# Performance work log

Hardware: AMD Instinct MI355X
Metric: run time of the kernel (lower is better)

## Reference

```python
import jax, jax.numpy as jnp
import numpy as np

B, N, D = 8, 1024, 768
R, SH = 10, 2
H = R + SH            # 12 total heads
DH = D // H           # 64
DF = 2 * D            # FFN hidden


def _layernorm(x, g, b, eps=1e-5):
    mu = jnp.mean(x, axis=-1, keepdims=True)
    var = jnp.var(x, axis=-1, keepdims=True)
    return (x - mu) * jax.lax.rsqrt(var + eps) * g + b


def setup_inputs() -> dict:
    key = jax.random.key(0)
    ks = jax.random.split(key, 12)
    s = 0.02
    inp = {
        'nodes': jax.random.normal(ks[0], (B, N, D), dtype=jnp.float32),
        'relation_mask': jax.random.uniform(ks[1], (B, N, N, R), dtype=jnp.float32),
        'node_mask': jax.random.randint(ks[2], (B, N), 0, 2).astype(bool),
        'Wq': jax.random.normal(ks[3], (D, D), dtype=jnp.float32) * s,
        'bq': jnp.zeros((D,), jnp.float32),
        'Wk': jax.random.normal(ks[4], (D, D), dtype=jnp.float32) * s,
        'bk': jnp.zeros((D,), jnp.float32),
        'Wv': jax.random.normal(ks[5], (D, D), dtype=jnp.float32) * s,
        'bv': jnp.zeros((D,), jnp.float32),
        'Wo': jax.random.normal(ks[6], (D, D), dtype=jnp.float32) * s,
        'bo': jnp.zeros((D,), jnp.float32),
        'ln1_g': jnp.ones((D,), jnp.float32),
        'ln1_b': jnp.zeros((D,), jnp.float32),
        'W1': jax.random.normal(ks[7], (DF, D), dtype=jnp.float32) * s,
        'b1': jnp.zeros((DF,), jnp.float32),
        'W2': jax.random.normal(ks[8], (D, DF), dtype=jnp.float32) * s,
        'b2': jnp.zeros((D,), jnp.float32),
        'ln2_g': jnp.ones((D,), jnp.float32),
        'ln2_b': jnp.zeros((D,), jnp.float32),
    }
    return inp


def reference(nodes, relation_mask, node_mask, Wq, bq, Wk, bk, Wv, bv, Wo, bo,
              ln1_g, ln1_b, W1, b1, W2, b2, ln2_g, ln2_b):
    neg_inf = jnp.float32(-jnp.inf)
    # projections -> [B, H, N, DH]
    q = (nodes @ Wq.T + bq).reshape(B, N, H, DH).transpose(0, 2, 1, 3)
    k = (nodes @ Wk.T + bk).reshape(B, N, H, DH).transpose(0, 2, 1, 3)
    v = (nodes @ Wv.T + bv).reshape(B, N, H, DH).transpose(0, 2, 1, 3)
    scores = jnp.einsum('bhqd,bhkd->bhqk', q, k) / jnp.sqrt(jnp.float32(DH))
    # relation-typed gating on first R heads
    rel_gate = relation_mask.transpose(0, 3, 1, 2)          # [B, R, N, N]
    typed = jnp.where(rel_gate < 1e-4, neg_inf, scores[:, :R])
    scores = jnp.concatenate([typed, scores[:, R:]], axis=1)
    # key padding mask
    key_mask = node_mask[:, None, None, :]                  # [B,1,1,N]
    scores = jnp.where(key_mask, scores, neg_inf)
    attn = jax.nn.softmax(scores, axis=-1)
    attn = jnp.nan_to_num(attn, nan=0.0)                    # rows with no valid keys -> 0
    out = jnp.einsum('bhqk,bhkd->bhqd', attn, v)
    out = out.transpose(0, 2, 1, 3).reshape(B, N, D)
    out = out @ Wo.T + bo
    h = _layernorm(nodes + out, ln1_g, ln1_b)
    ffn = jax.nn.gelu(h @ W1.T + b1, approximate=False) @ W2.T + b2
    h = _layernorm(h + ffn, ln2_g, ln2_b)
    return h
```

## Files before the change

kernel.cpp:

```cpp
#include <hip/hip_runtime.h>
#include <stdint.h>
#include <math.h>

typedef unsigned short u16;
typedef __bf16 bf16x8 __attribute__((ext_vector_type(8)));
typedef unsigned short u16x8 __attribute__((ext_vector_type(8)));
typedef unsigned short us4 __attribute__((ext_vector_type(4)));
typedef float f32x4 __attribute__((ext_vector_type(4)));

#define DEVI __device__ __forceinline__

constexpr int B_ = 8, N_ = 1024, D_ = 768, H_ = 12, DH_ = 64, DF_ = 1536;

DEVI u16 f2bu(float f) {
  unsigned x = __builtin_bit_cast(unsigned, f);
  x += 0x7FFFu + ((x >> 16) & 1u);
  return (u16)(x >> 16);
}
DEVI float b2f(u16 u) { return __builtin_bit_cast(float, (unsigned)u << 16); }

DEVI bf16x8 ld_frag(const u16* p) {
  return __builtin_bit_cast(bf16x8, *(const u16x8*)p);
}

DEVI void gload_lds16(const u16* g, u16* l) {
  __builtin_amdgcn_global_load_lds(
      (const __attribute__((address_space(1))) void*)g,
      (__attribute__((address_space(3))) void*)l, 16, 0, 0);
}

struct CvtArgs {
  const float* src[7];
  u16* dst[7];
  int n4[7];
  int start[8];
};
__global__ __launch_bounds__(256)
void cvt_all(CvtArgs a) {
  const int gb = blockIdx.x;
  int j = 0;
  while (gb >= a.start[j + 1]) ++j;
  const int i = (gb - a.start[j]) * 256 + threadIdx.x;
  if (i >= a.n4[j]) return;
  float4 v = ((const float4*)a.src[j])[i];
  ushort4 o;
  o.x = f2bu(v.x); o.y = f2bu(v.y); o.z = f2bu(v.z); o.w = f2bu(v.w);
  ((ushort4*)a.dst[j])[i] = o;
}

__global__ __launch_bounds__(256)
void build_mask_packed(const float* __restrict__ rel, const int* __restrict__ nm,
                       u16* __restrict__ mp) {
  const int b = blockIdx.z, q0 = blockIdx.y * 16, k0 = blockIdx.x * 256;
  const int t = threadIdx.x;
  __shared__ u16 w12[16][256];
  const int key_ok = nm[(b << 10) + k0 + t];
  const float th = 1e-4f;
#pragma unroll 1
  for (int it = 0; it < 16; ++it) {
    unsigned bits;
    if (!key_ok) {
      bits = 0xFFFu;
    } else {
      const size_t idx = (((size_t)(b << 10) + q0 + it) << 10) + k0 + t;
      const float2* rp = (const float2*)(rel + idx * 10);
      float2 a0 = rp[0], a1 = rp[1], a2 = rp[2], a3 = rp[3], a4 = rp[4];
      bits  = (a0.x < th ? 1u : 0u)   | (a0.y < th ? 2u : 0u)
            | (a1.x < th ? 4u : 0u)   | (a1.y < th ? 8u : 0u)
            | (a2.x < th ? 16u : 0u)  | (a2.y < th ? 32u : 0u)
            | (a3.x < th ? 64u : 0u)  | (a3.y < th ? 128u : 0u)
            | (a4.x < th ? 256u : 0u) | (a4.y < th ? 512u : 0u);
    }
    w12[it][t ^ ((it & 7) << 1)] = (u16)bits;
  }
  __syncthreads();
  const int ql = t & 15, kt = t >> 4;
  unsigned wv[16];
#pragma unroll
  for (int j2 = 0; j2 < 8; ++j2) {
    const int e = (kt * 16 + j2 * 2) ^ ((ql & 7) << 1);
    wv[j2 * 2] = w12[ql][e];
    wv[j2 * 2 + 1] = w12[ql][e + 1];
  }
#pragma unroll
  for (int h = 0; h < 12; ++h) {
    unsigned word = 0;
#pragma unroll
    for (int j = 0; j < 16; ++j) word |= ((wv[j] >> h) & 1u) << j;
    mp[(((size_t)(b * H_ + h)) * (N_ / 16) + (k0 >> 4) + kt) * N_ + q0 + ql] = (u16)word;
  }
}

template<int EPI>
__global__ __launch_bounds__(256, 2)
void gemm_bt(const u16* __restrict__ A, const u16* __restrict__ Bm,
             const float* __restrict__ bias0, const float* __restrict__ bias1,
             const float* __restrict__ residf, const u16* __restrict__ residb,
             u16* __restrict__ out0, u16* __restrict__ out1,
             int M, int N, int K) {
  __shared__ u16 As[2][128 * 32];
  __shared__ u16 Bs[2][128 * 32];
  const int t = threadIdx.x;
  const int w = t >> 6, l = t & 63;
  const int li = l & 15, grp = l >> 4;
  const int nwg = gridDim.x * gridDim.y;
  int id = blockIdx.y * gridDim.x + blockIdx.x;
  id = (id & 7) * (nwg >> 3) + (id >> 3);
  const int by = id / gridDim.x;
  const int bx = id - by * gridDim.x;
  const int n0 = bx * 128, m0 = by * 128;
  const int wr = w >> 1, wc = w & 1;

  f32x4 acc[4][4] = {};

  const int arow = w * 16 + (l >> 2);
  const int acol = (l & 3) * 8;
  const u16* Ag = A + (size_t)(m0 + arow) * K + acol;
  const u16* Bg = Bm + (size_t)(n0 + arow) * K + acol;

  auto stage = [&](int buf, int k0) {
    u16* Asw = &As[buf][(w * 16) * 32];
    u16* Bsw = &Bs[buf][(w * 16) * 32];
    gload_lds16(Ag + k0, Asw);
    gload_lds16(Ag + (size_t)64 * K + k0, Asw + 64 * 32);
    gload_lds16(Bg + k0, Bsw);
    gload_lds16(Bg + (size_t)64 * K + k0, Bsw + 64 * 32);
  };

  stage(0, 0);
  __syncthreads();
  int cur = 0;
  for (int k0 = 0; k0 < K; k0 += 32) {
    if (k0 + 32 < K) stage(cur ^ 1, k0 + 32);
    bf16x8 af[4], bfr[4];
#pragma unroll
    for (int m = 0; m < 4; ++m)
      af[m] = ld_frag(&As[cur][(wr * 64 + m * 16 + li) * 32 + grp * 8]);
#pragma unroll
    for (int n = 0; n < 4; ++n)
      bfr[n] = ld_frag(&Bs[cur][(wc * 64 + n * 16 + li) * 32 + grp * 8]);
#pragma unroll
    for (int m = 0; m < 4; ++m)
#pragma unroll
      for (int n = 0; n < 4; ++n)
        acc[m][n] = __builtin_amdgcn_mfma_f32_16x16x32_bf16(af[m], bfr[n], acc[m][n], 0, 0, 0);
    __syncthreads();
    cur ^= 1;
  }

#pragma unroll
  for (int m = 0; m < 4; ++m) {
#pragma unroll
    for (int n = 0; n < 4; ++n) {
#pragma unroll
      for (int j = 0; j < 4; ++j) {
        const int row = m0 + wr * 64 + m * 16 + grp * 4 + j;
        const int col = n0 + wc * 64 + n * 16 + li;
        float v = acc[m][n][j];
        if constexpr (EPI == 0) {
          v += (col < D_) ? bias0[col] : bias1[col - D_];
          if (col < D_) v *= 0.125f;
          const int b = row >> 10, i = row & (N_ - 1);
          int c2 = (col < D_) ? col : col - D_;
          u16* dst = (col < D_) ? out0 : out1;
          dst[(((size_t)(b * H_ + (c2 >> 6))) * N_ + i) * DH_ + (c2 & 63)] = f2bu(v);
        } else if constexpr (EPI == 1) {
          v += bias0[row];
          const int b = col >> 10, i = col & (N_ - 1);
          out0[(((size_t)(b * H_ + (row >> 6))) * DH_ + (row & 63)) * N_ + i] = f2bu(v);
        } else if constexpr (EPI == 2) {
          v += bias0[col] + residf[(size_t)row * N + col];
          out0[(size_t)row * N + col] = f2bu(v);
        } else if constexpr (EPI == 3) {
          v += bias0[col];
          float gel = 0.5f * v * (1.0f + erff(v * 0.70710678118654752440f));
          out0[(size_t)row * N + col] = f2bu(gel);
        } else {
          v += bias0[col] + b2f(residb[(size_t)row * N + col]);
          out0[(size_t)row * N + col] = f2bu(v);
        }
      }
    }
  }
}

__global__ __launch_bounds__(512, 4)
void attn(const u16* __restrict__ q, const u16* __restrict__ k, const u16* __restrict__ vT,
          const u16* __restrict__ mp, u16* __restrict__ outp) {
  const int nwg = gridDim.x;
  const int p = blockIdx.x;
  const int lid = (p & 7) * (nwg >> 3) + (p >> 3);
  const int bh_i = lid >> 3;
  const int qblk = lid & 7;
  const int b = bh_i / H_, h = bh_i - (bh_i / H_) * H_;
  const int w = threadIdx.x >> 6, l = threadIdx.x & 63;
  const int li = l & 15, grp = l >> 4;
  const int qw = qblk * 128 + w * 16;
  const size_t bh = (size_t)bh_i;

  __shared__ u16 Kt[2][64 * 64];
  __shared__ u16 Vt[2][64 * 64];
  __shared__ u16 P[8][16 * 64];

  const u16* kbase = k + bh * N_ * DH_;
  const u16* vbase = vT + bh * DH_ * N_;

  const int srow_off = l >> 3;
  const int sg = l & 7;
  const int r0 = w * 8;
  auto stageK = [&](int buf, int kj0) {
    const int row = r0 + srow_off;
    const int gp = sg ^ (row & 7);
    gload_lds16(kbase + (size_t)(kj0 + row) * DH_ + gp * 8, &Kt[buf][r0 * 64]);
  };
  auto stageV = [&](int buf, int kj0) {
    const int row = r0 + srow_off;
    const int gp = sg ^ (row & 7);
    gload_lds16(vbase + (size_t)row * N_ + kj0 + gp * 8, &Vt[buf][r0 * 64]);
  };

  const u16* qp = q + (bh * N_ + qw) * DH_;
  const bf16x8 bq0 = ld_frag(qp + li * DH_ + grp * 8);
  const bf16x8 bq1 = ld_frag(qp + li * DH_ + 32 + grp * 8);

  f32x4 accO[4] = {};
  float m = -INFINITY, lsum = 0.f;

  u16* Pw = &P[w][0];
  const int sw = (li & 7) << 3;
  const int prow = li * 64;
  const u16* mrow = mp + bh * (N_ / 16) * N_ + qw + li;

  stageK(0, 0); stageV(0, 0);
  __syncthreads();
  int cur = 0;

  for (int kj0 = 0; kj0 < N_; kj0 += 64) {
    if (kj0 + 64 < N_) { stageK(cur ^ 1, kj0 + 64); stageV(cur ^ 1, kj0 + 64); }
    unsigned mword[4];
#pragma unroll
    for (int t = 0; t < 4; ++t) mword[t] = mrow[(size_t)((kj0 >> 4) + t) * N_];

    f32x4 s[4];
    __builtin_amdgcn_s_setprio(1);
#pragma unroll
    for (int t = 0; t < 4; ++t) {
      const int row = t * 16 + li;
      const int rs = row & 7;
      const bf16x8 ka0 = ld_frag(&Kt[cur][row * 64 + ((grp ^ rs) * 8)]);
      const bf16x8 ka1 = ld_frag(&Kt[cur][row * 64 + (((grp + 4) ^ rs) * 8)]);
      f32x4 z = {0.f, 0.f, 0.f, 0.f};
      z = __builtin_amdgcn_mfma_f32_16x16x32_bf16(ka0, bq0, z, 0, 0, 0);
      z = __builtin_amdgcn_mfma_f32_16x16x32_bf16(ka1, bq1, z, 0, 0, 0);
      s[t] = z;
    }
    __builtin_amdgcn_s_setprio(0);

    float sv[16];
    float rmax = -INFINITY;
#pragma unroll
    for (int t = 0; t < 4; ++t) {
      const unsigned mb = (mword[t] >> (grp * 4)) & 0xFu;
#pragma unroll
      for (int j = 0; j < 4; ++j) {
        const float x = ((mb >> j) & 1u) ? -INFINITY : s[t][j];
        sv[t * 4 + j] = x;
        rmax = fmaxf(rmax, x);
      }
    }
    rmax = fmaxf(rmax, __shfl_xor(rmax, 16));
    rmax = fmaxf(rmax, __shfl_xor(rmax, 32));
    if (!__all(rmax <= m + 8.f)) {
      const float mnew = fmaxf(m, rmax);
      const float scal = (m == -INFINITY) ? 0.f : __expf(m - mnew);
      lsum *= scal;
#pragma unroll
      for (int t2 = 0; t2 < 4; ++t2) accO[t2] *= scal;
      m = mnew;
    }
    const float msafe = (m == -INFINITY) ? 0.f : m;
    float psum = 0.f;
    float pv[16];
#pragma unroll
    for (int i = 0; i < 16; ++i) {
      const float e = __expf(sv[i] - msafe);
      pv[i] = e;
      psum += e;
    }
    psum += __shfl_xor(psum, 16);
    psum += __shfl_xor(psum, 32);
    lsum += psum;
#pragma unroll
    for (int t = 0; t < 4; ++t) {
      us4 pk;
      pk[0] = f2bu(pv[t * 4 + 0]); pk[1] = f2bu(pv[t * 4 + 1]);
      pk[2] = f2bu(pv[t * 4 + 2]); pk[3] = f2bu(pv[t * 4 + 3]);
      *(us4*)&Pw[prow + ((t * 16 + grp * 4) ^ sw)] = pk;
    }
    __builtin_amdgcn_s_setprio(1);
#pragma unroll
    for (int kc = 0; kc < 2; ++kc) {
      const bf16x8 pb = ld_frag(&Pw[prow + ((kc * 32 + grp * 8) ^ sw)]);
#pragma unroll
      for (int t2 = 0; t2 < 4; ++t2) {
        const int row = t2 * 16 + li;
        const bf16x8 va = ld_frag(&Vt[cur][row * 64 + (((kc * 4 + grp) ^ (row & 7)) * 8)]);
        accO[t2] = __builtin_amdgcn_mfma_f32_16x16x32_bf16(va, pb, accO[t2], 0, 0, 0);
      }
    }
    __builtin_amdgcn_s_setprio(0);
    __syncthreads();
    cur ^= 1;
  }
  const float inv = (lsum > 0.f) ? 1.0f / lsum : 0.f;
  u16* op = outp + ((size_t)b * N_ + qw + li) * D_ + h * DH_;
#pragma unroll
  for (int t2 = 0; t2 < 4; ++t2) {
    us4 ov;
    ov[0] = f2bu(accO[t2][0] * inv); ov[1] = f2bu(accO[t2][1] * inv);
    ov[2] = f2bu(accO[t2][2] * inv); ov[3] = f2bu(accO[t2][3] * inv);
    *(us4*)&op[t2 * 16 + grp * 4] = ov;
  }
}

template<int OUTF32>
__global__ __launch_bounds__(256)
void ln_kernel(const u16* __restrict__ x, const float* __restrict__ g,
               const float* __restrict__ be, u16* __restrict__ ybf,
               float* __restrict__ yf) {
  const int row = blockIdx.x;
  const int t = threadIdx.x;
  const u16* xr = x + (size_t)row * D_;
  const float v0 = b2f(xr[t]), v1 = b2f(xr[t + 256]), v2 = b2f(xr[t + 512]);
  float s = v0 + v1 + v2;
  float s2 = v0 * v0 + v1 * v1 + v2 * v2;
#pragma unroll
  for (int d = 1; d < 64; d <<= 1) { s += __shfl_xor(s, d); s2 += __shfl_xor(s2, d); }
  __shared__ float red[8];
  const int w = t >> 6;
  if ((t & 63) == 0) { red[w] = s; red[4 + w] = s2; }
  __syncthreads();
  s = red[0] + red[1] + red[2] + red[3];
  s2 = red[4] + red[5] + red[6] + red[7];
  const float mu = s * (1.0f / D_);
  const float var = fmaxf(s2 * (1.0f / D_) - mu * mu, 0.0f);
  const float rstd = rsqrtf(var + 1e-5f);
#pragma unroll
  for (int c = 0; c < 3; ++c) {
    const int idx = t + c * 256;
    const float vv = (c == 0) ? v0 : (c == 1) ? v1 : v2;
    const float o = (vv - mu) * rstd * g[idx] + be[idx];
    if constexpr (OUTF32) yf[(size_t)row * D_ + idx] = o;
    else ybf[(size_t)row * D_ + idx] = f2bu(o);
  }
}

extern "C" void kernel_launch(void* const* d_in, const int* in_sizes, int n_in,
                              void* d_out, int out_size, void* d_ws, size_t ws_size,
                              hipStream_t stream) {
  (void)in_sizes; (void)n_in; (void)out_size; (void)ws_size;
  const float* nodes = (const float*)d_in[0];
  const float* rel   = (const float*)d_in[1];
  const int*   nmask = (const int*)d_in[2];
  const float* Wq = (const float*)d_in[3];
  const float* bq = (const float*)d_in[4];
  const float* Wk = (const float*)d_in[5];
  const float* bk = (const float*)d_in[6];
  const float* Wv = (const float*)d_in[7];
  const float* bv = (const float*)d_in[8];
  const float* Wo = (const float*)d_in[9];
  const float* bo = (const float*)d_in[10];
  const float* ln1g = (const float*)d_in[11];
  const float* ln1b = (const float*)d_in[12];
  const float* W1 = (const float*)d_in[13];
  const float* b1 = (const float*)d_in[14];
  const float* W2 = (const float*)d_in[15];
  const float* b2 = (const float*)d_in[16];
  const float* ln2g = (const float*)d_in[17];
  const float* ln2b = (const float*)d_in[18];
  float* out = (float*)d_out;

  char* ws = (char*)d_ws;
  u16* Wqk_bf = (u16*)(ws + 0);
  u16* Wv_bf  = (u16*)(ws + 2359296);
  u16* Wo_bf  = (u16*)(ws + 3538944);
  u16* W1_bf  = (u16*)(ws + 4718592);
  u16* W2_bf  = (u16*)(ws + 7077888);
  u16* Xbf    = (u16*)(ws + 9437184);
  u16* qb     = (u16*)(ws + 22020096);
  u16* kb     = (u16*)(ws + 34603008);
  u16* vTb    = (u16*)(ws + 47185920);
  u16* mwb    = (u16*)(ws + 59768832);
  u16* prehb  = (u16*)(ws + 22020096);
  u16* hbf    = (u16*)(ws + 47185920);
  u16* f1b    = (u16*)(ws + 59768832);
  u16* preob  = (u16*)(ws + 84934656);
  u16* attno  = Xbf;

  const dim3 blk(256);
  build_mask_packed<<<dim3(4, 64, 8), blk, 0, stream>>>(rel, nmask, mwb);
  CvtArgs ca;
  ca.src[0] = Wq; ca.src[1] = Wk; ca.src[2] = Wv; ca.src[3] = Wo;
  ca.src[4] = W1; ca.src[5] = W2; ca.src[6] = nodes;
  ca.dst[0] = Wqk_bf; ca.dst[1] = Wqk_bf + 768 * 768; ca.dst[2] = Wv_bf;
  ca.dst[3] = Wo_bf; ca.dst[4] = W1_bf; ca.dst[5] = W2_bf; ca.dst[6] = Xbf;
  ca.n4[0] = ca.n4[1] = ca.n4[2] = ca.n4[3] = 147456;
  ca.n4[4] = ca.n4[5] = 294912; ca.n4[6] = 1572864;
  ca.start[0] = 0; ca.start[1] = 576; ca.start[2] = 1152; ca.start[3] = 1728;
  ca.start[4] = 2304; ca.start[5] = 3456; ca.start[6] = 4608; ca.start[7] = 10752;
  cvt_all<<<10752, blk, 0, stream>>>(ca);
  gemm_bt<0><<<dim3(12, 64), blk, 0, stream>>>(Xbf, Wqk_bf, bq, bk, nullptr, nullptr,
                                               qb, kb, 8192, 1536, 768);
  gemm_bt<1><<<dim3(64, 6), blk, 0, stream>>>(Wv_bf, Xbf, bv, nullptr, nullptr, nullptr,
                                              vTb, nullptr, 768, 8192, 768);
  attn<<<768, dim3(512), 0, stream>>>(qb, kb, vTb, mwb, attno);
  gemm_bt<2><<<dim3(6, 64), blk, 0, stream>>>(attno, Wo_bf, bo, nullptr, nodes, nullptr,
                                              prehb, nullptr, 8192, 768, 768);
  ln_kernel<0><<<8192, blk, 0, stream>>>(prehb, ln1g, ln1b, hbf, nullptr);
  gemm_bt<3><<<dim3(12, 64), blk, 0, stream>>>(hbf, W1_bf, b1, nullptr, nullptr, nullptr,
                                               f1b, nullptr, 8192, 1536, 768);
  gemm_bt<4><<<dim3(6, 64), blk, 0, stream>>>(f1b, W2_bf, b2, nullptr, nullptr, hbf,
                                              preob, nullptr, 8192, 768, 1536);
  ln_kernel<1><<<8192, blk, 0, stream>>>(preob, ln2g, ln2b, nullptr, out);
}
```

Measured before the change: 307.4 us.

## Add 256x256 triple-buffered GEMM, fuse QKV projection into one launch

Adds a new 512-thread GEMM kernel with 256x256 tiles, a three-stage LDS pipeline, prefetch interleaved with MFMA blocks, and s_setprio around the MFMA sections. The Q, K and V projections are merged into a single GEMM over a concatenated weight, with the epilogue routing columns to the q, k or transposed-v layouts. The FFN1 GELU GEMM also moves to the new kernel. The aim is more data reuse per tile and fewer launches. In exchange, the grids are small (288 and 192 workgroups on a GPU with many CUs), and the V output is now written transposed from a row-major tile, so those stores are strided.

Measured after the change: 380.7 us. +23.9%, slower.

```diff
diff --git a/kernel.cpp b/kernel.cpp
--- a/kernel.cpp
+++ b/kernel.cpp
@@ -92,11 +92,132 @@
 }
 
 template<int EPI>
+__global__ __launch_bounds__(512, 2)
+void gemm256(const u16* __restrict__ A, const u16* __restrict__ Bm,
+             const float* __restrict__ bia0, const float* __restrict__ bia1,
+             const float* __restrict__ bia2,
+             u16* __restrict__ o0, u16* __restrict__ o1, u16* __restrict__ o2,
+             int N) {
+  constexpr int K = 768, NT = 24;
+  __shared__ u16 As[3][256 * 32];
+  __shared__ u16 Bs[3][256 * 32];
+  const int t = threadIdx.x;
+  const int w = t >> 6, l = t & 63;
+  const int li = l & 15, grp = l >> 4;
+  const int wr = w >> 2, wc = w & 3;
+
+  const int nbx = N >> 8;
+  const int nwg = gridDim.x;
+  int id = blockIdx.x;
+  id = (id & 7) * (nwg >> 3) + (id >> 3);
+  const int by = id / nbx, bx = id - by * nbx;
+  const int m0 = by * 256, n0 = bx * 256;
+
+  const int srl = t >> 2;
+  const int sg = t & 3;
+  auto stA = [&](int buf, int kt) {
+#pragma unroll
+    for (int i = 0; i < 2; ++i) {
+      const int rl = i * 128 + srl;
+      const int gs = sg ^ ((rl >> 2) & 3);
+      gload_lds16(A + (size_t)(m0 + rl) * K + kt * 32 + gs * 8,
+                  &As[buf][i * 4096 + w * 512]);
+    }
+  };
+  auto stB = [&](int buf, int kt) {
+#pragma unroll
+    for (int i = 0; i < 2; ++i) {
+      const int rl = i * 128 + srl;
+      const int gs = sg ^ ((rl >> 2) & 3);
+      gload_lds16(Bm + (size_t)(n0 + rl) * K + kt * 32 + gs * 8,
+                  &Bs[buf][i * 4096 + w * 512]);
+    }
+  };
+  auto rdA = [&](int buf, int fm) -> bf16x8 {
+    const int row = wr * 128 + fm * 16 + li;
+    const int g = grp ^ ((row >> 2) & 3);
+    return ld_frag(&As[buf][row * 32 + g * 8]);
+  };
+  auto rdB = [&](int buf, int n) -> bf16x8 {
+    const int row = wc * 64 + n * 16 + li;
+    const int g = grp ^ ((row >> 2) & 3);
+    return ld_frag(&Bs[buf][row * 32 + g * 8]);
+  };
+
+  f32x4 acc[8][4] = {};
+
+  stA(0, 0); stB(0, 0); stA(1, 1); stB(1, 1);
+  asm volatile("s_waitcnt vmcnt(4)\n\ts_barrier" ::: "memory");
+
+  for (int kt = 0; kt < NT; ++kt) {
+    const int bt = kt % 3, b2 = (kt + 2) % 3;
+    const bool pre = (kt + 2 < NT);
+    if (pre) stA(b2, kt + 2);
+    bf16x8 bfr[4], af[4];
+#pragma unroll
+    for (int n = 0; n < 4; ++n) bfr[n] = rdB(bt, n);
+#pragma unroll
+    for (int fm = 0; fm < 4; ++fm) af[fm] = rdA(bt, fm);
+    __builtin_amdgcn_s_setprio(1);
+#pragma unroll
+    for (int fm = 0; fm < 4; ++fm)
+#pragma unroll
+      for (int n = 0; n < 4; ++n)
+        acc[fm][n] = __builtin_amdgcn_mfma_f32_16x16x32_bf16(af[fm], bfr[n], acc[fm][n], 0, 0, 0);
+    __builtin_amdgcn_s_setprio(0);
+    if (pre) stB(b2, kt + 2);
+#pragma unroll
+    for (int fm = 0; fm < 4; ++fm) af[fm] = rdA(bt, fm + 4);
+    __builtin_amdgcn_s_setprio(1);
+#pragma unroll
+    for (int fm = 0; fm < 4; ++fm)
+#pragma unroll
+      for (int n = 0; n < 4; ++n)
+        acc[fm + 4][n] = __builtin_amdgcn_mfma_f32_16x16x32_bf16(af[fm], bfr[n], acc[fm + 4][n], 0, 0, 0);
+    __builtin_amdgcn_s_setprio(0);
+    if (pre) asm volatile("s_waitcnt vmcnt(4)\n\ts_barrier" ::: "memory");
+    else     asm volatile("s_waitcnt vmcnt(0)\n\ts_barrier" ::: "memory");
+  }
+
+#pragma unroll
+  for (int fm = 0; fm < 8; ++fm) {
+#pragma unroll
+    for (int n = 0; n < 4; ++n) {
+      const int col = n0 + wc * 64 + n * 16 + li;
+#pragma unroll
+      for (int j = 0; j < 4; ++j) {
+        const int row = m0 + wr * 128 + fm * 16 + grp * 4 + j;
+        float v = acc[fm][n][j];
+        if constexpr (EPI == 0) {
+          const int b = row >> 10, i = row & (N_ - 1);
+          if (col < D_) {
+            v = (v + bia0[col]) * 0.125f;
+            o0[(((size_t)(b * H_ + (col >> 6))) * N_ + i) * DH_ + (col & 63)] = f2bu(v);
+          } else if (col < 2 * D_) {
+            const int c = col - D_;
+            v += bia1[c];
+            o1[(((size_t)(b * H_ + (c >> 6))) * N_ + i) * DH_ + (c & 63)] = f2bu(v);
+          } else {
+            const int c = col - 2 * D_;
+            v += bia2[c];
+            o2[(((size_t)(b * H_ + (c >> 6))) * DH_ + (c & 63)) * N_ + i] = f2bu(v);
+          }
+        } else {
+          v += bia0[col];
+          float gel = 0.5f * v * (1.0f + erff(v * 0.70710678118654752440f));
+          o0[(size_t)row * N + col] = f2bu(gel);
+        }
+      }
+    }
+  }
+}
+
+template<int EPI>
 __global__ __launch_bounds__(256, 2)
 void gemm_bt(const u16* __restrict__ A, const u16* __restrict__ Bm,
-             const float* __restrict__ bias0, const float* __restrict__ bias1,
+             const float* __restrict__ bias0,
              const float* __restrict__ residf, const u16* __restrict__ residb,
-             u16* __restrict__ out0, u16* __restrict__ out1,
+             u16* __restrict__ out0,
              int M, int N, int K) {
   __shared__ u16 As[2][128 * 32];
   __shared__ u16 Bs[2][128 * 32];
@@ -157,24 +278,9 @@
         const int row = m0 + wr * 64 + m * 16 + grp * 4 + j;
         const int col = n0 + wc * 64 + n * 16 + li;
         float v = acc[m][n][j];
-        if constexpr (EPI == 0) {
-          v += (col < D_) ? bias0[col] : bias1[col - D_];
-          if (col < D_) v *= 0.125f;
-          const int b = row >> 10, i = row & (N_ - 1);
-          int c2 = (col < D_) ? col : col - D_;
-          u16* dst = (col < D_) ? out0 : out1;
-          dst[(((size_t)(b * H_ + (c2 >> 6))) * N_ + i) * DH_ + (c2 & 63)] = f2bu(v);
-        } else if constexpr (EPI == 1) {
-          v += bias0[row];
-          const int b = col >> 10, i = col & (N_ - 1);
-          out0[(((size_t)(b * H_ + (row >> 6))) * DH_ + (row & 63)) * N_ + i] = f2bu(v);
-        } else if constexpr (EPI == 2) {
+        if constexpr (EPI == 2) {
           v += bias0[col] + residf[(size_t)row * N + col];
           out0[(size_t)row * N + col] = f2bu(v);
-        } else if constexpr (EPI == 3) {
-          v += bias0[col];
-          float gel = 0.5f * v * (1.0f + erff(v * 0.70710678118654752440f));
-          out0[(size_t)row * N + col] = f2bu(gel);
         } else {
           v += bias0[col] + b2f(residb[(size_t)row * N + col]);
           out0[(size_t)row * N + col] = f2bu(v);
@@ -381,8 +487,7 @@
   float* out = (float*)d_out;
 
   char* ws = (char*)d_ws;
-  u16* Wqk_bf = (u16*)(ws + 0);
-  u16* Wv_bf  = (u16*)(ws + 2359296);
+  u16* Wqkv_bf = (u16*)(ws + 0);
   u16* Wo_bf  = (u16*)(ws + 3538944);
   u16* W1_bf  = (u16*)(ws + 4718592);
   u16* W2_bf  = (u16*)(ws + 7077888);
@@ -402,24 +507,22 @@
   CvtArgs ca;
   ca.src[0] = Wq; ca.src[1] = Wk; ca.src[2] = Wv; ca.src[3] = Wo;
   ca.src[4] = W1; ca.src[5] = W2; ca.src[6] = nodes;
-  ca.dst[0] = Wqk_bf; ca.dst[1] = Wqk_bf + 768 * 768; ca.dst[2] = Wv_bf;
+  ca.dst[0] = Wqkv_bf; ca.dst[1] = Wqkv_bf + 768 * 768; ca.dst[2] = Wqkv_bf + 2 * 768 * 768;
   ca.dst[3] = Wo_bf; ca.dst[4] = W1_bf; ca.dst[5] = W2_bf; ca.dst[6] = Xbf;
   ca.n4[0] = ca.n4[1] = ca.n4[2] = ca.n4[3] = 147456;
   ca.n4[4] = ca.n4[5] = 294912; ca.n4[6] = 1572864;
   ca.start[0] = 0; ca.start[1] = 576; ca.start[2] = 1152; ca.start[3] = 1728;
   ca.start[4] = 2304; ca.start[5] = 3456; ca.start[6] = 4608; ca.start[7] = 10752;
   cvt_all<<<10752, blk, 0, stream>>>(ca);
-  gemm_bt<0><<<dim3(12, 64), blk, 0, stream>>>(Xbf, Wqk_bf, bq, bk, nullptr, nullptr,
-                                               qb, kb, 8192, 1536, 768);
-  gemm_bt<1><<<dim3(64, 6), blk, 0, stream>>>(Wv_bf, Xbf, bv, nullptr, nullptr, nullptr,
-                                              vTb, nullptr, 768, 8192, 768);
+  gemm256<0><<<288, dim3(512), 0, stream>>>(Xbf, Wqkv_bf, bq, bk, bv,
+                                            qb, kb, vTb, 2304);
   attn<<<768, dim3(512), 0, stream>>>(qb, kb, vTb, mwb, attno);
-  gemm_bt<2><<<dim3(6, 64), blk, 0, stream>>>(attno, Wo_bf, bo, nullptr, nodes, nullptr,
-                                              prehb, nullptr, 8192, 768, 768);
+  gemm_bt<2><<<dim3(6, 64), blk, 0, stream>>>(attno, Wo_bf, bo, nodes, nullptr,
+                                              prehb, 8192, 768, 768);
   ln_kernel<0><<<8192, blk, 0, stream>>>(prehb, ln1g, ln1b, hbf, nullptr);
-  gemm_bt<3><<<dim3(12, 64), blk, 0, stream>>>(hbf, W1_bf, b1, nullptr, nullptr, nullptr,
-                                               f1b, nullptr, 8192, 1536, 768);
-  gemm_bt<4><<<dim3(6, 64), blk, 0, stream>>>(f1b, W2_bf, b2, nullptr, nullptr, hbf,
-                                              preob, nullptr, 8192, 768, 1536);
+  gemm256<1><<<192, dim3(512), 0, stream>>>(hbf, W1_bf, b1, nullptr, nullptr,
+                                            f1b, nullptr, nullptr, 1536);
+  gemm_bt<4><<<dim3(6, 64), blk, 0, stream>>>(f1b, W2_bf, b2, nullptr, hbf,
+                                              preob, 8192, 768, 1536);
   ln_kernel<1><<<8192, blk, 0, stream>>>(preob, ln2g, ln2b, nullptr, out);
 }
```
